# Optimization experiments

Measured on AMD Instinct MI355X. Metric: run time of the kernel, lower is better.

The kernel has to match this reference:

```python
import jax, jax.numpy as jnp
import numpy as np

B, S, D, H = 128, 512, 512, 4
DH = D // H

def setup_inputs() -> dict:
    key = jax.random.key(0)
    ks = jax.random.split(key, 12)
    s = 1.0 / np.sqrt(D)
    inp = {
        "x": jax.random.normal(ks[0], (B, S, D), dtype=jnp.float32),
        "Wi": jax.random.uniform(ks[1], (D, D), jnp.float32, -s, s),
        "bi": jnp.zeros((D,), jnp.float32),
        "Wq": jax.random.uniform(ks[2], (D, D), jnp.float32, -s, s),
        "bq": jnp.zeros((D,), jnp.float32),
        "Wk": jax.random.uniform(ks[3], (D, D), jnp.float32, -s, s),
        "bk": jnp.zeros((D,), jnp.float32),
        "Wv": jax.random.uniform(ks[4], (D, D), jnp.float32, -s, s),
        "bv": jnp.zeros((D,), jnp.float32),
        "Wo": jax.random.uniform(ks[5], (D, D), jnp.float32, -s, s),
        "bo": jnp.zeros((D,), jnp.float32),
        "data_lens": jax.random.randint(ks[6], (B,), 1, S + 1, dtype=jnp.int32),
    }
    return inp


def _forward(x, Wi, bi, Wq, bq, Wk, bk, Wv, bv, Wo, bo, data_lens):
    # fc_i applied to the whole sequence up front
    xf = x @ Wi + bi                      # [B, S, D]
    h0 = xf[:, 0, :]                      # initial state = fc_i(x)[:, 0]
    scale = 1.0 / jnp.sqrt(jnp.asarray(DH, xf.dtype))

    def step(h, x_t):
        # h: [B, D] previous state (acts as key and value, kv_len == 1)
        # x_t: [B, D] current input (query)
        q = (x_t @ Wq + bq).reshape(B, H, DH)
        k = (h @ Wk + bk).reshape(B, H, DH)
        v = (h @ Wv + bv).reshape(B, H, DH)
        scores = jnp.sum(q * k, axis=-1, keepdims=True) * scale   # [B, H, 1]
        w = jax.nn.softmax(scores, axis=-1)                       # == 1 (single key)
        attn = (w * v).reshape(B, D)
        h_new = attn @ Wo + bo + x_t                              # residual
        return h_new, h_new

    xs = jnp.transpose(xf, (1, 0, 2))     # [S, B, D]
    _, outs = jax.lax.scan(step, h0, xs)  # [S, B, D]
    outputs = jnp.transpose(outs, (1, 0, 2))                      # [B, S, D]

    idx = (data_lens.astype(jnp.int32) - 1)[:, None, None]        # [B,1,1]
    final_state = jnp.take_along_axis(outputs, idx, axis=1)[:, 0, :]
    return outputs, final_state


def reference(x, Wi, bi, Wq, bq, Wk, bk, Wv, bv, Wo, bo, data_lens):
    return _forward(x, Wi, bi, Wq, bq, Wk, bk, Wv, bv, Wo, bo, data_lens)
```

## Files before the change

### kernel.cpp

```cpp
#include <hip/hip_runtime.h>
#include <hip/hip_bf16.h>

typedef __hip_bfloat16 bf16;
typedef __attribute__((ext_vector_type(8))) short short8;
typedef __attribute__((ext_vector_type(4))) float f32x4;

#define S_LEN 512
#define DIM   512
#define BATCH 128
#define ROWS  (BATCH * S_LEN)

__device__ inline unsigned short f2bu(float f){
    bf16 h = __float2bfloat16(f);
    return *reinterpret_cast<unsigned short*>(&h);
}
__device__ inline float ld_in(const void* p, size_t i, int f32){
    return f32 ? ((const float*)p)[i] : __bfloat162float(((const bf16*)p)[i]);
}

typedef __attribute__((address_space(1))) const unsigned int gu32;
typedef __attribute__((address_space(3))) unsigned int lu32;
__device__ __forceinline__ void gld16(const void* g, void* l){
    __builtin_amdgcn_global_load_lds((gu32*)g, (lu32*)l, 16, 0, 0);
}

__device__ __forceinline__ short8 lds_frag(const unsigned short* base, int row, int koff){
    const unsigned off = ((unsigned)(row*128 + koff*2)) ^ (((unsigned)(row & 7)) << 4);
    return *(const short8*)((const char*)base + off);
}

__global__ void detect_dtype(const unsigned int* __restrict__ x, int* __restrict__ flag)
{
    __shared__ int cnt;
    if (threadIdx.x == 0) cnt = 0;
    __syncthreads();
    int loc = 0;
    for (int i = threadIdx.x; i < 8192; i += 256)
        if (((x[i] >> 7) & 0xFFu) == 0xFFu) loc++;
    atomicAdd(&cnt, loc);
    __syncthreads();
    if (threadIdx.x == 0) *flag = (cnt > 0) ? 1 : 0;
}

__global__ void conv_tr(const void* __restrict__ in, bf16* __restrict__ outp,
                        const int* __restrict__ flagp)
{
    const int f32 = *flagp;
    __shared__ unsigned short tile[32][33];
    const int bx = blockIdx.x, by = blockIdx.y;
    const int tx = threadIdx.x, ty = threadIdx.y;
    #pragma unroll
    for (int j = 0; j < 32; j += 8)
        tile[ty + j][tx] = f2bu(ld_in(in, (size_t)(by*32 + ty + j)*DIM + bx*32 + tx, f32));
    __syncthreads();
    #pragma unroll
    for (int j = 0; j < 32; j += 8) {
        unsigned short u = tile[tx][ty + j];
        outp[(size_t)(bx*32 + ty + j)*DIM + by*32 + tx] = *reinterpret_cast<bf16*>(&u);
    }
}

__global__ void conv_cp(const void* __restrict__ in, bf16* __restrict__ outp,
                        const int* __restrict__ flagp)
{
    const int f32 = *flagp;
    const size_t i = (size_t)blockIdx.x*256 + threadIdx.x;
    outp[i] = __float2bfloat16(ld_in(in, i, f32));
}

__global__ void conv_x(const void* __restrict__ X, size_t eoff, bf16* __restrict__ xb,
                       const int* __restrict__ flagp)
{
    const int f32 = *flagp;
    const size_t i = ((size_t)blockIdx.x*256 + threadIdx.x)*8;
    if (f32) {
        const float* p = (const float*)X + eoff + i;
        float4 a = *(const float4*)p;
        float4 b = *(const float4*)(p + 4);
        __align__(16) unsigned short wv[8];
        wv[0]=f2bu(a.x); wv[1]=f2bu(a.y); wv[2]=f2bu(a.z); wv[3]=f2bu(a.w);
        wv[4]=f2bu(b.x); wv[5]=f2bu(b.y); wv[6]=f2bu(b.z); wv[7]=f2bu(b.w);
        *(uint4*)(xb + i) = *(const uint4*)wv;
    } else {
        *(uint4*)(xb + i) = *(const uint4*)((const bf16*)X + eoff + i);
    }
}

__global__ void cvec_kernel(const bf16* __restrict__ WoT, const void* __restrict__ bv,
                            const void* __restrict__ bo, const void* __restrict__ bi,
                            const int* __restrict__ flagp,
                            float* __restrict__ dvec, float* __restrict__ bvec)
{
    const int f32 = *flagp;
    const int n = blockIdx.x * 4 + (threadIdx.x >> 6);
    const int lane = threadIdx.x & 63;
    float acc = 0.f;
    for (int k = lane; k < DIM; k += 64)
        acc += ld_in(bv, k, f32) * __bfloat162float(WoT[(size_t)n*DIM + k]);
    #pragma unroll
    for (int o = 32; o > 0; o >>= 1) acc += __shfl_down(acc, o, 64);
    if (lane == 0) {
        const float dd = acc + ld_in(bo, n, f32);
        dvec[n] = dd;
        bvec[n] = dd + ld_in(bi, n, f32);
    }
}

__global__ void prep_aux(const float* __restrict__ U0, const float* __restrict__ V0,
                         const float* __restrict__ dvec,
                         bf16* __restrict__ A1, bf16* __restrict__ V0b, bf16* __restrict__ Zr)
{
    const int idx = blockIdx.x * 256 + threadIdx.x;
    const int n = idx & 511;
    A1[idx]  = __float2bfloat16(U0[idx] - dvec[n]);
    V0b[idx] = __float2bfloat16(V0[idx]);
    if (idx < 512) Zr[idx] = __float2bfloat16(0.f);
}

#define TILE_PROLOGUE                                                          \
    __shared__ __align__(16) unsigned short As[128][72];                       \
    __shared__ __align__(16) unsigned short Bs[128][72];                       \
    const int tid  = threadIdx.x;                                              \
    const int lane = tid & 63;                                                 \
    const int wave = tid >> 6;                                                 \
    const int wm = (wave & 1) * 64;                                            \
    const int wn = (wave >> 1) * 64;                                           \
    const int cn = lane & 15;                                                  \
    const int quad = lane >> 4;                                                \
    f32x4 acc[4][4];                                                           \
    _Pragma("unroll")                                                          \
    for (int i = 0; i < 4; ++i)                                                \
        _Pragma("unroll")                                                      \
        for (int j = 0; j < 4; ++j) acc[i][j] = (f32x4){0.f,0.f,0.f,0.f};

#define TILE_MFMA                                                              \
        __syncthreads();                                                       \
        _Pragma("unroll")                                                      \
        for (int ks = 0; ks < 64; ks += 32) {                                  \
            short8 af[4], bfr[4];                                              \
            const int koff = ks + quad*8;                                      \
            _Pragma("unroll")                                                  \
            for (int i = 0; i < 4; ++i) af[i]  = *(const short8*)&As[wm + i*16 + cn][koff]; \
            _Pragma("unroll")                                                  \
            for (int j = 0; j < 4; ++j) bfr[j] = *(const short8*)&Bs[wn + j*16 + cn][koff]; \
            _Pragma("unroll")                                                  \
            for (int i = 0; i < 4; ++i)                                        \
                _Pragma("unroll")                                              \
                for (int j = 0; j < 4; ++j)                                    \
                    acc[i][j] = __builtin_amdgcn_mfma_f32_16x16x32_bf16(af[i], bfr[j], acc[i][j], 0, 0, 0); \
        }                                                                      \
        __syncthreads();

#define STAGE_B(Bt, C0)                                                        \
        {                                                                      \
            int r = tid >> 3; const int c = (tid & 7) * 8;                     \
            _Pragma("unroll")                                                  \
            for (int p = 0; p < 4; ++p, r += 32) {                             \
                uint4 v = *(const uint4*)((Bt) + (size_t)((C0) + r)*DIM + k0 + c); \
                *(uint4*)&Bs[r][c] = v;                                        \
            }                                                                  \
        }

#define STAGE_A_IN(SRC, BASE)                                                  \
                if (f32) {                                                     \
                    const float* sp = (const float*)(SRC) + (BASE);            \
                    float4 a = *(const float4*)sp;                             \
                    float4 b = *(const float4*)(sp + 4);                       \
                    __align__(16) unsigned short w[8];                         \
                    w[0]=f2bu(a.x); w[1]=f2bu(a.y); w[2]=f2bu(a.z); w[3]=f2bu(a.w); \
                    w[4]=f2bu(b.x); w[5]=f2bu(b.y); w[6]=f2bu(b.z); w[7]=f2bu(b.w); \
                    *(uint4*)&As[r][c] = *(const uint4*)w;                     \
                } else {                                                       \
                    *(uint4*)&As[r][c] = *(const uint4*)((const bf16*)(SRC) + (BASE)); \
                }

__global__ __launch_bounds__(256) void gemm_sq(const bf16* __restrict__ A,
        const bf16* __restrict__ Btm, bf16* __restrict__ Pout, bf16* __restrict__ Tout)
{
    TILE_PROLOGUE
    const int R0 = blockIdx.y * 128;
    const int C0 = blockIdx.x * 128;
    for (int k0 = 0; k0 < DIM; k0 += 64) {
        {
            int r = tid >> 3; const int c = (tid & 7) * 8;
            #pragma unroll
            for (int p = 0; p < 4; ++p, r += 32)
                *(uint4*)&As[r][c] = *(const uint4*)(A + (size_t)(R0 + r)*DIM + k0 + c);
        }
        STAGE_B(Btm, C0)
        TILE_MFMA
    }
    #pragma unroll
    for (int i = 0; i < 4; ++i) {
        const int rowb = R0 + wm + i*16 + quad*4;
        #pragma unroll
        for (int j = 0; j < 4; ++j) {
            const int cc = C0 + wn + j*16 + cn;
            #pragma unroll
            for (int rr = 0; rr < 4; ++rr) {
                const float v = acc[i][j][rr];
                Pout[(size_t)(rowb + rr)*DIM + cc] = __float2bfloat16(v);
                Tout[(size_t)cc*DIM + rowb + rr]  = __float2bfloat16(v);
            }
        }
    }
}

__global__ __launch_bounds__(256) void gemm_row0(const void* __restrict__ X,
        const bf16* __restrict__ WiT, const float* __restrict__ bvec,
        const int* __restrict__ flagp, float* __restrict__ U0)
{
    const int f32 = *flagp;
    TILE_PROLOGUE
    const int C0 = blockIdx.x * 128;
    for (int k0 = 0; k0 < DIM; k0 += 64) {
        {
            int r = tid >> 3; const int c = (tid & 7) * 8;
            #pragma unroll
            for (int p = 0; p < 4; ++p, r += 32) {
                const size_t base = (size_t)r*S_LEN*DIM + k0 + c;
                STAGE_A_IN(X, base)
            }
        }
        STAGE_B(WiT, C0)
        TILE_MFMA
    }
    #pragma unroll
    for (int i = 0; i < 4; ++i) {
        const int rowb = wm + i*16 + quad*4;
        #pragma unroll
        for (int j = 0; j < 4; ++j) {
            const int cc = C0 + wn + j*16 + cn;
            const float bb = bvec[cc];
            #pragma unroll
            for (int rr = 0; rr < 4; ++rr)
                U0[(size_t)(rowb + rr)*DIM + cc] = acc[i][j][rr] + bb;
        }
    }
}

__global__ __launch_bounds__(256) void gemm_v0(const float* __restrict__ U0,
        const bf16* __restrict__ T0, const float* __restrict__ dvec, float* __restrict__ V0)
{
    TILE_PROLOGUE
    const int C0 = blockIdx.x * 128;
    for (int k0 = 0; k0 < DIM; k0 += 64) {
        {
            int r = tid >> 3; const int c = (tid & 7) * 8;
            #pragma unroll
            for (int p = 0; p < 4; ++p, r += 32) {
                __align__(16) unsigned short w[8];
                #pragma unroll
                for (int q = 0; q < 8; ++q)
                    w[q] = f2bu(U0[(size_t)r*DIM + k0 + c + q] - dvec[k0 + c + q]);
                *(uint4*)&As[r][c] = *(const uint4*)w;
            }
        }
        STAGE_B(T0, C0)
        TILE_MFMA
    }
    #pragma unroll
    for (int i = 0; i < 4; ++i) {
        const int rowb = wm + i*16 + quad*4;
        #pragma unroll
        for (int j = 0; j < 4; ++j) {
            const int cc = C0 + wn + j*16 + cn;
            #pragma unroll
            for (int rr = 0; rr < 4; ++rr) {
                const size_t off = (size_t)(rowb + rr)*DIM + cc;
                V0[off] = acc[i][j][rr] + U0[off];
            }
        }
    }
}

template<int MODE, bool TO_OUT>
__global__ __launch_bounds__(256, 2) void gemm_big(
        const bf16* __restrict__ Abf, const bf16* __restrict__ A1,
        const bf16* __restrict__ V0b, const bf16* __restrict__ Zr,
        const bf16* __restrict__ Bt,  const float* __restrict__ Rf,
        float* __restrict__ Of, bf16* __restrict__ Ob,
        void* __restrict__ Oout, size_t eoff, const int* __restrict__ flagp,
        const int shift)
{
    __shared__ __align__(16) unsigned short As[2][128*64];
    __shared__ __align__(16) unsigned short Bs[2][128*64];
    const int tid  = threadIdx.x;
    const int lane = tid & 63;
    const int w    = tid >> 6;
    const int nb = gridDim.x;
    const int p0 = blockIdx.x;
    const int L  = (p0 & 7) * (nb >> 3) + (p0 >> 3);
    const int bx = L & 3, by = L >> 2;
    const int R0 = by * 128, C0 = bx * 128;
    const int wm = (w & 1) * 64;
    const int wn = (w >> 1) * 64;
    const int cn = lane & 15;
    const int quad = lane >> 4;
    f32x4 acc[4][4];
    #pragma unroll
    for (int i = 0; i < 4; ++i)
        #pragma unroll
        for (int j = 0; j < 4; ++j) acc[i][j] = (f32x4){0.f,0.f,0.f,0.f};

    const int lr  = w*8 + (lane >> 3);
    const int lcb = ((lane & 7) ^ (lane >> 3)) * 8;
    const bf16* aln[4];
    const bf16* bln[4];
    #pragma unroll
    for (int l = 0; l < 4; ++l) {
        const int r    = l*32 + lr;
        const int grow = R0 + r;
        const bf16* a;
        if (MODE == 2) {
            a = Abf + (size_t)grow*DIM;
        } else if (MODE == 1) {
            const int t = grow & (S_LEN - 1);
            if      (t == 0) a = A1  + (size_t)(grow >> 9)*DIM;
            else if (t == 1) a = V0b + (size_t)(grow >> 9)*DIM;
            else             a = Abf + (size_t)(grow - 1)*DIM;
        } else {
            const int t = grow & (S_LEN - 1);
            a = (t >= shift) ? (Abf + (size_t)(grow - shift)*DIM) : Zr;
        }
        aln[l] = a + lcb;
        bln[l] = Bt + (size_t)(C0 + r)*DIM + lcb;
    }

    {
        unsigned short* Ad = &As[0][0];
        unsigned short* Bd = &Bs[0][0];
        gld16(aln[0], Ad + 0*2048 + w*512);
        gld16(aln[2], Ad + 2*2048 + w*512);
        gld16(bln[0], Bd + 0*2048 + w*512);
        gld16(bln[2], Bd + 2*2048 + w*512);
        gld16(aln[1], Ad + 1*2048 + w*512);
        gld16(aln[3], Ad + 3*2048 + w*512);
        gld16(bln[1], Bd + 1*2048 + w*512);
        gld16(bln[3], Bd + 3*2048 + w*512);
    }
    asm volatile("s_waitcnt vmcnt(4)" ::: "memory");
    __builtin_amdgcn_s_barrier();

#define PHASE(MQ, NQ, STAGEA, L0, L1, DOWAIT)                                   \
    {                                                                           \
        short8 af0 = lds_frag(&As[cur][0], wm + (MQ)*32 +  0 + cn,      quad*8);\
        short8 af1 = lds_frag(&As[cur][0], wm + (MQ)*32 + 16 + cn,      quad*8);\
        short8 af2 = lds_frag(&As[cur][0], wm + (MQ)*32 +  0 + cn, 32 + quad*8);\
        short8 af3 = lds_frag(&As[cur][0], wm + (MQ)*32 + 16 + cn, 32 + quad*8);\
        short8 bg0 = lds_frag(&Bs[cur][0], wn + (NQ)*32 +  0 + cn,      quad*8);\
        short8 bg1 = lds_frag(&Bs[cur][0], wn + (NQ)*32 + 16 + cn,      quad*8);\
        short8 bg2 = lds_frag(&Bs[cur][0], wn + (NQ)*32 +  0 + cn, 32 + quad*8);\
        short8 bg3 = lds_frag(&Bs[cur][0], wn + (NQ)*32 + 16 + cn, 32 + quad*8);\
        if (STAGEA) {                                                           \
            gld16(aln[L0] + knt, Ad + (L0)*2048 + w*512);                       \
            gld16(aln[L1] + knt, Ad + (L1)*2048 + w*512);                       \
        } else {                                                                \
            gld16(bln[L0] + knt, Bd + (L0)*2048 + w*512);                       \
            gld16(bln[L1] + knt, Bd + (L1)*2048 + w*512);                       \
        }                                                                       \
        __builtin_amdgcn_s_barrier();                                           \
        __builtin_amdgcn_s_setprio(1);                                          \
        acc[(MQ)*2+0][(NQ)*2+0] = __builtin_amdgcn_mfma_f32_16x16x32_bf16(af0, bg0, acc[(MQ)*2+0][(NQ)*2+0], 0, 0, 0); \
        acc[(MQ)*2+1][(NQ)*2+0] = __builtin_amdgcn_mfma_f32_16x16x32_bf16(af1, bg0, acc[(MQ)*2+1][(NQ)*2+0], 0, 0, 0); \
        acc[(MQ)*2+0][(NQ)*2+1] = __builtin_amdgcn_mfma_f32_16x16x32_bf16(af0, bg1, acc[(MQ)*2+0][(NQ)*2+1], 0, 0, 0); \
        acc[(MQ)*2+1][(NQ)*2+1] = __builtin_amdgcn_mfma_f32_16x16x32_bf16(af1, bg1, acc[(MQ)*2+1][(NQ)*2+1], 0, 0, 0); \
        acc[(MQ)*2+0][(NQ)*2+0] = __builtin_amdgcn_mfma_f32_16x16x32_bf16(af2, bg2, acc[(MQ)*2+0][(NQ)*2+0], 0, 0, 0); \
        acc[(MQ)*2+1][(NQ)*2+0] = __builtin_amdgcn_mfma_f32_16x16x32_bf16(af3, bg2, acc[(MQ)*2+1][(NQ)*2+0], 0, 0, 0); \
        acc[(MQ)*2+0][(NQ)*2+1] = __builtin_amdgcn_mfma_f32_16x16x32_bf16(af2, bg3, acc[(MQ)*2+0][(NQ)*2+1], 0, 0, 0); \
        acc[(MQ)*2+1][(NQ)*2+1] = __builtin_amdgcn_mfma_f32_16x16x32_bf16(af3, bg3, acc[(MQ)*2+1][(NQ)*2+1], 0, 0, 0); \
        __builtin_amdgcn_s_setprio(0);                                          \
        if (DOWAIT) asm volatile("s_waitcnt vmcnt(4)" ::: "memory");            \
        __builtin_amdgcn_s_barrier();                                           \
    }

    #pragma unroll
    for (int kt = 0; kt < 8; ++kt) {
        const int cur = kt & 1;
        const int knt = ((kt + 1) & 7) * 64;
        unsigned short* Ad = &As[cur ^ 1][0];
        unsigned short* Bd = &Bs[cur ^ 1][0];
        PHASE(0, 0, true,  0, 2, 1)
        PHASE(1, 0, false, 0, 2, 1)
        PHASE(0, 1, true,  1, 3, 0)
        PHASE(1, 1, false, 1, 3, 1)
    }
#undef PHASE
    asm volatile("s_waitcnt vmcnt(0)" ::: "memory");

    const int f32o = TO_OUT ? *flagp : 0;
    #pragma unroll
    for (int i = 0; i < 4; ++i) {
        const int rowb = R0 + wm + i*16 + quad*4;
        #pragma unroll
        for (int j = 0; j < 4; ++j) {
            const int cc = C0 + wn + j*16 + cn;
            #pragma unroll
            for (int rr = 0; rr < 4; ++rr) {
                const size_t off = (size_t)(rowb + rr)*DIM + cc;
                const float res = (MODE == 2) ? Rf[cc] : Rf[off];
                const float v = acc[i][j][rr] + res;
                if (TO_OUT) {
                    if (f32o) ((float*)Oout)[eoff + off] = v;
                    else      ((bf16*)Oout)[eoff + off]  = __float2bfloat16(v);
                } else {
                    Of[off] = v;
                    Ob[off] = __float2bfloat16(v);
                }
            }
        }
    }
}

__global__ void gather_final(void* __restrict__ out, const int* __restrict__ lens,
                             const int* __restrict__ flagp)
{
    const int f32 = *flagp;
    const int idx = blockIdx.x * 256 + threadIdx.x;
    const int b = idx >> 9, n = idx & 511;
    int L = lens[b];
    if (L < 1) L = 1;
    if (L > S_LEN) L = S_LEN;
    const size_t src = ((size_t)b*S_LEN + (L - 1))*DIM + n;
    const size_t dst = (size_t)ROWS*DIM + idx;
    if (f32) ((float*)out)[dst] = ((const float*)out)[src];
    else     ((bf16*)out)[dst]  = ((const bf16*)out)[src];
}

extern "C" void kernel_launch(void* const* d_in, const int* in_sizes, int n_in,
                              void* d_out, int out_size, void* d_ws, size_t ws_size,
                              hipStream_t stream)
{
    const void* X  = d_in[0];
    const void* Wi = d_in[1];
    const void* bi = d_in[2];
    const void* Wv = d_in[7];
    const void* bv = d_in[8];
    const void* Wo = d_in[9];
    const void* bo = d_in[10];
    const int* lens = (const int*)d_in[11];
    char* ws = (char*)d_ws;

    const size_t MATB = (size_t)DIM * DIM * sizeof(bf16);
    bf16* WiT = (bf16*)(ws + 0*MATB);
    bf16* WoT = (bf16*)(ws + 1*MATB);
    bf16* Wvb = (bf16*)(ws + 2*MATB);
    bf16* S2  = (bf16*)(ws + 3*MATB);
    bf16* S3  = (bf16*)(ws + 4*MATB);
    bf16* T0  = (bf16*)(ws + 5*MATB);
    bf16* T1  = (bf16*)(ws + 6*MATB);
    bf16* T2  = (bf16*)(ws + 7*MATB);
    bf16* T3  = (bf16*)(ws + 8*MATB);
    size_t off = 9*MATB;
    float* dvec = (float*)(ws + off); off += 2048;
    float* bvec = (float*)(ws + off); off += 2048;
    int*   flag = (int*)  (ws + off); off += 256;
    float* U0   = (float*)(ws + off); off += (size_t)BATCH*DIM*4;
    float* V0   = (float*)(ws + off); off += (size_t)BATCH*DIM*4;
    bf16*  A1   = (bf16*) (ws + off); off += (size_t)BATCH*DIM*2;
    bf16*  V0b  = (bf16*) (ws + off); off += (size_t)BATCH*DIM*2;
    bf16*  Zr   = (bf16*) (ws + off); off += 1024;
    off = (off + 1023) & ~(size_t)1023;
    char* dyn = ws + off;
    const size_t avail = ws_size > off ? ws_size - off : 0;

    int CR = 512;
    for (long cr = 65536; cr >= 512; cr >>= 1)
        if ((size_t)cr * 7168 <= avail) { CR = (int)cr; break; }

    bf16*  xbf = (bf16*) dyn;
    float* Uf  = (float*)(dyn + (size_t)CR*1024);
    bf16*  Ub  = (bf16*) (dyn + (size_t)CR*3072);
    float* Vf  = (float*)(dyn + (size_t)CR*4096);
    bf16*  Vb  = (bf16*) (dyn + (size_t)CR*6144);

    detect_dtype<<<1, 256, 0, stream>>>((const unsigned int*)X, flag);
    conv_tr<<<dim3(16,16), dim3(32,8), 0, stream>>>(Wi, WiT, flag);
    conv_tr<<<dim3(16,16), dim3(32,8), 0, stream>>>(Wo, WoT, flag);
    conv_cp<<<1024, 256, 0, stream>>>(Wv, Wvb, flag);
    cvec_kernel<<<128, 256, 0, stream>>>(WoT, bv, bo, bi, flag, dvec, bvec);
    gemm_sq<<<dim3(4,4), 256, 0, stream>>>(Wvb, WoT, S2, T0);
    gemm_sq<<<dim3(4,4), 256, 0, stream>>>(S2, T0, S3, T1);
    gemm_sq<<<dim3(4,4), 256, 0, stream>>>(S3, T1, S2, T2);
    gemm_sq<<<dim3(4,4), 256, 0, stream>>>(S2, T2, S3, T3);
    gemm_row0<<<dim3(4,1), 256, 0, stream>>>(X, WiT, bvec, flag, U0);
    gemm_v0<<<dim3(4,1), 256, 0, stream>>>(U0, T0, dvec, V0);
    prep_aux<<<256, 256, 0, stream>>>(U0, V0, dvec, A1, V0b, Zr);

    const int NC = ROWS / CR;
    const int RT = CR / 128;
    const int nb = 4 * RT;
    for (int c = 0; c < NC; ++c) {
        const size_t eoff = (size_t)c*CR*DIM;
        const size_t boff = (size_t)(c*(CR/S_LEN))*DIM;
        conv_x<<<CR/4, 256, 0, stream>>>(X, eoff, xbf, flag);
        gemm_big<2,false><<<nb, 256, 0, stream>>>(xbf, nullptr, nullptr, Zr,
                WiT, bvec, Uf, Ub, nullptr, 0, flag, 0);
        gemm_big<1,false><<<nb, 256, 0, stream>>>(Ub, A1 + boff, V0b + boff, Zr,
                T0, Uf, Vf, Vb, nullptr, 0, flag, 1);
        gemm_big<0,false><<<nb, 256, 0, stream>>>(Vb, nullptr, nullptr, Zr,
                T1, Vf, Uf, Ub, nullptr, 0, flag, 2);
        gemm_big<0,false><<<nb, 256, 0, stream>>>(Ub, nullptr, nullptr, Zr,
                T2, Uf, Vf, Vb, nullptr, 0, flag, 4);
        gemm_big<0,true ><<<nb, 256, 0, stream>>>(Vb, nullptr, nullptr, Zr,
                T3, Vf, nullptr, nullptr, d_out, eoff, flag, 8);
    }
    gather_final<<<256, 256, 0, stream>>>(d_out, lens, flag);
}
```

Before: 1.016 ms.

## Add 256x256-tile double-buffered GEMM kernel for two middle doubling stages

Adds a new GEMM kernel with 256x256 output tiles, 512 threads and 128KB of dynamic LDS, double-buffering A and B tiles through direct global-to-LDS loads interleaved with MFMA groups. It is used for the two mode-0 shifted-residual GEMM stages in place of the 128-row tile kernel. Larger tiles raise arithmetic intensity and cut redundant loads of A and B, but mean fewer blocks (CR/128) and higher LDS and register pressure, which may lower occupancy.

```diff
diff --git a/kernel.cpp b/kernel.cpp
--- a/kernel.cpp
+++ b/kernel.cpp
@@ -412,6 +412,158 @@
     }
 }
 
+__global__ __launch_bounds__(512, 2) void gemm_256(
+        const bf16* __restrict__ Abf, const bf16* __restrict__ Zr,
+        const bf16* __restrict__ Bt,  const float* __restrict__ Rf,
+        float* __restrict__ Of, bf16* __restrict__ Ob, const int shift)
+{
+    extern __shared__ __align__(16) unsigned short smem[];
+    unsigned short* Ab0 = smem;
+    unsigned short* Ab1 = smem + 16384;
+    unsigned short* Bb0 = smem + 32768;
+    unsigned short* Bb1 = smem + 49152;
+
+    const int tid  = threadIdx.x;
+    const int lane = tid & 63;
+    const int w    = tid >> 6;
+    const int nb = gridDim.x;
+    const int p0 = blockIdx.x;
+    const int L  = ((nb & 7) == 0) ? ((p0 & 7) * (nb >> 3) + (p0 >> 3)) : p0;
+    const int bx = L & 1, by = L >> 1;
+    const int R0 = by * 256, C0 = bx * 256;
+    const int wr = w >> 2, wc = w & 3;
+    const int cn = lane & 15, quad = lane >> 4;
+
+    f32x4 acc[8][4];
+    #pragma unroll
+    for (int i = 0; i < 8; ++i)
+        #pragma unroll
+        for (int j = 0; j < 4; ++j) acc[i][j] = (f32x4){0.f,0.f,0.f,0.f};
+
+    const int lrow = w*8 + (lane >> 3);
+    const int scol = ((lane & 7) ^ (lane >> 3)) * 8;
+    const int ldst = w * 512;
+    const bf16* bl0 = Bt + (size_t)(C0 + lrow)*DIM + scol;
+    const bf16* aln[4];
+    #pragma unroll
+    for (int l = 0; l < 4; ++l) {
+        const int grow = R0 + l*64 + lrow;
+        const int t = grow & (S_LEN - 1);
+        const bf16* a = (t >= shift) ? (Abf + (size_t)(grow - shift)*DIM) : Zr;
+        aln[l] = a + scol;
+    }
+
+    gld16(bl0 + 0*64*DIM, Bb0 + 0*4096 + ldst);
+    gld16(bl0 + 1*64*DIM, Bb0 + 1*4096 + ldst);
+    gld16(bl0 + 2*64*DIM, Bb0 + 2*4096 + ldst);
+    gld16(bl0 + 3*64*DIM, Bb0 + 3*4096 + ldst);
+    gld16(aln[0], Ab0 + 0*4096 + ldst);
+    gld16(aln[2], Ab0 + 2*4096 + ldst);
+    gld16(aln[1], Ab0 + 1*4096 + ldst);
+    gld16(aln[3], Ab0 + 3*4096 + ldst);
+    asm volatile("s_waitcnt vmcnt(2)" ::: "memory");
+    __builtin_amdgcn_s_barrier();
+
+#define MFMA16(Q)                                                              \
+    __builtin_amdgcn_s_setprio(1);                                             \
+    _Pragma("unroll")                                                          \
+    for (int n = 0; n < 4; ++n) {                                              \
+        acc[(Q)*2+0][n] = __builtin_amdgcn_mfma_f32_16x16x32_bf16(x0, bg0[n], acc[(Q)*2+0][n], 0, 0, 0); \
+        acc[(Q)*2+1][n] = __builtin_amdgcn_mfma_f32_16x16x32_bf16(x1, bg0[n], acc[(Q)*2+1][n], 0, 0, 0); \
+    }                                                                          \
+    _Pragma("unroll")                                                          \
+    for (int n = 0; n < 4; ++n) {                                              \
+        acc[(Q)*2+0][n] = __builtin_amdgcn_mfma_f32_16x16x32_bf16(x2, bg1[n], acc[(Q)*2+0][n], 0, 0, 0); \
+        acc[(Q)*2+1][n] = __builtin_amdgcn_mfma_f32_16x16x32_bf16(x3, bg1[n], acc[(Q)*2+1][n], 0, 0, 0); \
+    }                                                                          \
+    __builtin_amdgcn_s_setprio(0);
+
+#define RDA(Q, KH) \
+    x0 = lds_frag(Ac, wr*128 + ((Q)*2+0)*16 + cn, (KH)*32 + quad*8);           \
+    x1 = lds_frag(Ac, wr*128 + ((Q)*2+1)*16 + cn, (KH)*32 + quad*8);
+
+#define RDA4(Q)                                                                \
+    x0 = lds_frag(Ac, wr*128 + ((Q)*2+0)*16 + cn,      quad*8);                \
+    x1 = lds_frag(Ac, wr*128 + ((Q)*2+1)*16 + cn,      quad*8);                \
+    x2 = lds_frag(Ac, wr*128 + ((Q)*2+0)*16 + cn, 32 + quad*8);                \
+    x3 = lds_frag(Ac, wr*128 + ((Q)*2+1)*16 + cn, 32 + quad*8);
+
+    for (int kt = 0; kt < 7; ++kt) {
+        const int knt = (kt + 1) << 6;
+        unsigned short* Ac = (kt & 1) ? Ab1 : Ab0;
+        unsigned short* Bc = (kt & 1) ? Bb1 : Bb0;
+        unsigned short* An = (kt & 1) ? Ab0 : Ab1;
+        unsigned short* Bn = (kt & 1) ? Bb0 : Bb1;
+        short8 bg0[4], bg1[4];
+        short8 x0, x1, x2, x3;
+        #pragma unroll
+        for (int n = 0; n < 4; ++n) {
+            bg0[n] = lds_frag(Bc, wc*64 + n*16 + cn,      quad*8);
+            bg1[n] = lds_frag(Bc, wc*64 + n*16 + cn, 32 + quad*8);
+        }
+        RDA4(0)
+        gld16(bl0 + 0*64*DIM + knt, Bn + 0*4096 + ldst);
+        gld16(bl0 + 1*64*DIM + knt, Bn + 1*4096 + ldst);
+        MFMA16(0)
+        RDA4(1)
+        gld16(bl0 + 2*64*DIM + knt, Bn + 2*4096 + ldst);
+        gld16(bl0 + 3*64*DIM + knt, Bn + 3*4096 + ldst);
+        MFMA16(1)
+        asm volatile("s_waitcnt vmcnt(4)" ::: "memory");
+        __builtin_amdgcn_s_barrier();
+        RDA4(2)
+        gld16(aln[0] + knt, An + 0*4096 + ldst);
+        gld16(aln[2] + knt, An + 2*4096 + ldst);
+        MFMA16(2)
+        RDA4(3)
+        gld16(aln[1] + knt, An + 1*4096 + ldst);
+        gld16(aln[3] + knt, An + 3*4096 + ldst);
+        MFMA16(3)
+        asm volatile("s_waitcnt vmcnt(2)" ::: "memory");
+        __builtin_amdgcn_s_barrier();
+    }
+    {
+        unsigned short* Ac = Ab1;
+        unsigned short* Bc = Bb1;
+        short8 bg0[4], bg1[4];
+        short8 x0, x1, x2, x3;
+        #pragma unroll
+        for (int n = 0; n < 4; ++n) {
+            bg0[n] = lds_frag(Bc, wc*64 + n*16 + cn,      quad*8);
+            bg1[n] = lds_frag(Bc, wc*64 + n*16 + cn, 32 + quad*8);
+        }
+        RDA4(0)
+        MFMA16(0)
+        RDA4(1)
+        MFMA16(1)
+        asm volatile("s_waitcnt vmcnt(0)" ::: "memory");
+        __builtin_amdgcn_s_barrier();
+        RDA4(2)
+        MFMA16(2)
+        RDA4(3)
+        MFMA16(3)
+    }
+#undef MFMA16
+#undef RDA
+#undef RDA4
+
+    #pragma unroll
+    for (int i = 0; i < 8; ++i) {
+        const int rowb = R0 + wr*128 + i*16 + quad*4;
+        #pragma unroll
+        for (int j = 0; j < 4; ++j) {
+            const int cc = C0 + wc*64 + j*16 + cn;
+            #pragma unroll
+            for (int rr = 0; rr < 4; ++rr) {
+                const size_t off = (size_t)(rowb + rr)*DIM + cc;
+                const float v = acc[i][j][rr] + Rf[off];
+                Of[off] = v;
+                Ob[off] = __float2bfloat16(v);
+            }
+        }
+    }
+}
+
 __global__ void gather_final(void* __restrict__ out, const int* __restrict__ lens,
                              const int* __restrict__ flagp)
 {
@@ -474,6 +626,9 @@
     float* Vf  = (float*)(dyn + (size_t)CR*4096);
     bf16*  Vb  = (bf16*) (dyn + (size_t)CR*6144);
 
+    hipFuncSetAttribute(reinterpret_cast<const void*>(gemm_256),
+                        hipFuncAttributeMaxDynamicSharedMemorySize, 131072);
+
     detect_dtype<<<1, 256, 0, stream>>>((const unsigned int*)X, flag);
     conv_tr<<<dim3(16,16), dim3(32,8), 0, stream>>>(Wi, WiT, flag);
     conv_tr<<<dim3(16,16), dim3(32,8), 0, stream>>>(Wo, WoT, flag);
@@ -490,6 +645,7 @@
     const int NC = ROWS / CR;
     const int RT = CR / 128;
     const int nb = 4 * RT;
+    const int nb256 = CR / 128;
     for (int c = 0; c < NC; ++c) {
         const size_t eoff = (size_t)c*CR*DIM;
         const size_t boff = (size_t)(c*(CR/S_LEN))*DIM;
@@ -498,10 +654,8 @@
                 WiT, bvec, Uf, Ub, nullptr, 0, flag, 0);
         gemm_big<1,false><<<nb, 256, 0, stream>>>(Ub, A1 + boff, V0b + boff, Zr,
                 T0, Uf, Vf, Vb, nullptr, 0, flag, 1);
-        gemm_big<0,false><<<nb, 256, 0, stream>>>(Vb, nullptr, nullptr, Zr,
-                T1, Vf, Uf, Ub, nullptr, 0, flag, 2);
-        gemm_big<0,false><<<nb, 256, 0, stream>>>(Ub, nullptr, nullptr, Zr,
-                T2, Uf, Vf, Vb, nullptr, 0, flag, 4);
+        gemm_256<<<nb256, 512, 131072, stream>>>(Vb, Zr, T1, Vf, Uf, Ub, 2);
+        gemm_256<<<nb256, 512, 131072, stream>>>(Ub, Zr, T2, Uf, Vf, Vb, 4);
         gemm_big<0,true ><<<nb, 256, 0, stream>>>(Vb, nullptr, nullptr, Zr,
                 T3, Vf, nullptr, nullptr, d_out, eoff, flag, 8);
     }
```

After: 993.8 us. -2.2%, faster.
